# Kernel optimization log

Hardware: AMD Instinct MI355X
Metric: run time of the kernel (lower is better)

The kernel has to match this reference:

```python
import jax, jax.numpy as jnp
import numpy as np

N = 50000
E = 800000
IN_DIM = 6
HID = 32
HEADS = 2
NEG_SLOPE = 0.2


def setup_inputs() -> dict:
    key = jax.random.key(0)
    ks = jax.random.split(key, 12)
    x = jax.random.normal(ks[0], (N, IN_DIM), dtype=jnp.float32)
    edge_index = jax.random.randint(ks[1], (2, E), 0, N, dtype=jnp.int64)
    s = 0.1
    W1 = jax.random.normal(ks[2], (IN_DIM, HEADS * HID), jnp.float32) * s
    a_src1 = jax.random.normal(ks[3], (HEADS, HID), jnp.float32) * s
    a_dst1 = jax.random.normal(ks[4], (HEADS, HID), jnp.float32) * s
    b1 = jnp.zeros((HEADS * HID,), jnp.float32)
    W2 = jax.random.normal(ks[5], (HEADS * HID, HID), jnp.float32) * s
    a_src2 = jax.random.normal(ks[6], (1, HID), jnp.float32) * s
    a_dst2 = jax.random.normal(ks[7], (1, HID), jnp.float32) * s
    b2 = jnp.zeros((HID,), jnp.float32)
    Wout = jax.random.normal(ks[8], (HID, 1), jnp.float32) * s
    bout = jnp.zeros((1,), jnp.float32)
    return {"x": x, "edge_index": edge_index, "W1": W1, "a_src1": a_src1,
            "a_dst1": a_dst1, "b1": b1, "W2": W2, "a_src2": a_src2,
            "a_dst2": a_dst2, "b2": b2, "Wout": Wout, "bout": bout}


def gat_conv(x, src, dst, n, W, a_src, a_dst, b, heads, out_ch, concat):
    # x: [N, F_in]; src/dst: [E'] (self-loops already appended)
    h = (x @ W).reshape(n, heads, out_ch)              # [N, H, C]
    alpha_s = jnp.sum(h * a_src, axis=-1)              # [N, H]
    alpha_d = jnp.sum(h * a_dst, axis=-1)              # [N, H]
    e = jax.nn.leaky_relu(alpha_s[src] + alpha_d[dst], NEG_SLOPE)  # [E', H]
    # segment softmax over incoming edges of each destination node
    m = jax.ops.segment_max(e, dst, num_segments=n)    # [N, H]
    ex = jnp.exp(e - m[dst])
    denom = jax.ops.segment_sum(ex, dst, num_segments=n)
    alpha = ex / denom[dst]                            # [E', H]
    out = jax.ops.segment_sum(alpha[:, :, None] * h[src], dst, num_segments=n)  # [N, H, C]
    out = out.reshape(n, heads * out_ch) if concat else out.mean(axis=1)
    return out + b


def reference(x, edge_index, W1, a_src1, a_dst1, b1, W2, a_src2, a_dst2, b2, Wout, bout):
    n = x.shape[0]
    loops = jnp.arange(n, dtype=edge_index.dtype)
    src = jnp.concatenate([edge_index[0], loops])
    dst = jnp.concatenate([edge_index[1], loops])
    h = jax.nn.relu(gat_conv(x, src, dst, n, W1, a_src1, a_dst1, b1, HEADS, HID, True))
    h = jax.nn.relu(gat_conv(h, src, dst, n, W2, a_src2, a_dst2, b2, 1, HID, False))
    return jax.nn.sigmoid(h @ Wout + bout).squeeze(-1)  # [N]
```

## Files before the change

### kernel.cpp

```cpp
#include <hip/hip_runtime.h>
#include <hip/hip_fp16.h>

#define N_NODES 50000
#define N_EDGES 800000
#define ETOT    (N_EDGES + N_NODES)
#define NEG_SLOPE 0.2f
#define NBIN    ((N_NODES + 255) / 256)
#define CHUNK   4096
#define B_COARSE ((ETOT + CHUNK - 1) / CHUNK)
#define G_NODE1 ((N_NODES + 3) / 4)
#define NG1     (N_NODES / 16)

__device__ __forceinline__ float leaky(float v) {
    return v > 0.f ? v : NEG_SLOPE * v;
}

__device__ __forceinline__ void edge_src_dst(const int* ei, int e, int& src, int& dst) {
    if (e < N_EDGES) { src = ei[e]; dst = ei[N_EDGES + e]; }
    else             { src = dst = e - N_EDGES; }
}

__global__ void k_pre(const float* __restrict__ x, const float* __restrict__ W1,
                      const float* __restrict__ a_src1, const float* __restrict__ a_dst1,
                      float* __restrict__ as1, float* __restrict__ ad1,
                      const int* __restrict__ ei, int* __restrict__ bh) {
    __shared__ int h[NBIN];
    if (blockIdx.x < G_NODE1) {
        int node = blockIdx.x * 4 + (threadIdx.x >> 6);
        if (node >= N_NODES) return;
        int j = threadIdx.x & 63;
        int head = j >> 5;
        float hv = 0.f;
#pragma unroll
        for (int k = 0; k < 6; ++k)
            hv += x[node * 6 + k] * W1[k * 64 + j];
        float s = hv * a_src1[j];
        float d = hv * a_dst1[j];
#pragma unroll
        for (int m = 1; m < 32; m <<= 1) {
            s += __shfl_xor(s, m);
            d += __shfl_xor(d, m);
        }
        if ((j & 31) == 0) {
            as1[node * 2 + head] = s;
            ad1[node * 2 + head] = d;
        }
    } else {
        int b = blockIdx.x - G_NODE1;
        for (int i = threadIdx.x; i < NBIN; i += 256) h[i] = 0;
        __syncthreads();
        int base = b * CHUNK;
        int lim = min(base + CHUNK, ETOT);
        for (int e = base + threadIdx.x; e < lim; e += 256) {
            int s, d; edge_src_dst(ei, e, s, d);
            atomicAdd(&h[d >> 8], 1);
        }
        __syncthreads();
        for (int i = threadIdx.x; i < NBIN; i += 256)
            bh[b * NBIN + i] = h[i];
    }
}

__global__ void k_cscan(int* __restrict__ bh, int* __restrict__ binoff) {
    __shared__ int s[256];
    int t = threadIdx.x;
    int run = 0;
    if (t < NBIN) {
        for (int b = 0; b < B_COARSE; ++b) {
            int v = bh[b * NBIN + t];
            bh[b * NBIN + t] = run;
            run += v;
        }
    }
    int v = (t < NBIN) ? run : 0;
    int x = v;
    s[t] = x;
    __syncthreads();
#pragma unroll
    for (int o = 1; o < 256; o <<= 1) {
        int tt = (t >= o) ? s[t - o] : 0;
        __syncthreads();
        x += tt;
        s[t] = x;
        __syncthreads();
    }
    if (t < NBIN) binoff[t] = x - v;
    if (t == 255) binoff[NBIN] = x;
}

__global__ void k_cscatter(const int* __restrict__ ei, const int* __restrict__ bh,
                           const int* __restrict__ binoff, unsigned* __restrict__ ebin) {
    __shared__ int cur[NBIN];
    for (int i = threadIdx.x; i < NBIN; i += 256)
        cur[i] = bh[blockIdx.x * NBIN + i] + binoff[i];
    __syncthreads();
    int base = blockIdx.x * CHUNK;
    int lim = min(base + CHUNK, ETOT);
    for (int e = base + threadIdx.x; e < lim; e += 256) {
        int s, d; edge_src_dst(ei, e, s, d);
        int pos = atomicAdd(&cur[d >> 8], 1);
        ebin[pos] = ((unsigned)s << 8) | (unsigned)(d & 255);
    }
}

__global__ void k_fine(const unsigned* __restrict__ ebin, const int* __restrict__ binoff,
                       int* __restrict__ rowstart, int* __restrict__ csr_src) {
    __shared__ int h[256];
    __shared__ int cur[256];
    int bin = blockIdx.x;
    int beg = binoff[bin], end = binoff[bin + 1];
    int t = threadIdx.x;
    h[t] = 0;
    __syncthreads();
    for (int i = beg + t; i < end; i += 256)
        atomicAdd(&h[ebin[i] & 255u], 1);
    __syncthreads();
    int v = h[t];
    int x = v;
    cur[t] = x;
    __syncthreads();
#pragma unroll
    for (int o = 1; o < 256; o <<= 1) {
        int tt = (t >= o) ? cur[t - o] : 0;
        __syncthreads();
        x += tt;
        cur[t] = x;
        __syncthreads();
    }
    int start = beg + x - v;
    int node = bin * 256 + t;
    if (node < N_NODES) rowstart[node] = start;
    if (bin == NBIN - 1 && t == 0) rowstart[N_NODES] = ETOT;
    cur[t] = start;
    __syncthreads();
    for (int i = beg + t; i < end; i += 256) {
        unsigned p = ebin[i];
        int pos = atomicAdd(&cur[p & 255u], 1);
        csr_src[pos] = (int)(p >> 8);
    }
}

__global__ void k_gat12(const int* __restrict__ csr_src, const int* __restrict__ rowstart,
                        const float* __restrict__ as1, const float* __restrict__ ad1,
                        const float* __restrict__ x, const float* __restrict__ W1,
                        const float* __restrict__ b1, const float* __restrict__ W2,
                        const float* __restrict__ as_w2, const float* __restrict__ ad_w2,
                        __half* __restrict__ h2h, float* __restrict__ as2,
                        float* __restrict__ ad2) {
    __shared__ float W2s[64 * 32];
    __shared__ float o1s[16 * 66];
    int t = threadIdx.x;
    for (int i = t; i < 64 * 32; i += 256)
        W2s[i] = W2[i];

    int l = t & 15;
    int ln = t >> 4;
    int node = blockIdx.x * 16 + ln;

    float p[4][6];
    float bv[4];
#pragma unroll
    for (int m = 0; m < 4; ++m) {
        int c = l + 16 * m;
#pragma unroll
        for (int k = 0; k < 6; ++k)
            p[m][k] = W1[k * 64 + c];
        bv[m] = b1[c];
    }

    int beg = rowstart[node], end = rowstart[node + 1];
    float2 adv = ((const float2*)ad1)[node];

    float a0 = 0, a1 = 0, a2 = 0, a3 = 0, a4 = 0, a5 = 0;
    float c0 = 0, c1 = 0, c2 = 0, c3 = 0, c4 = 0, c5 = 0;
    float dp0 = 0, dp1 = 0;
    for (int i = beg + l; i < end; i += 16) {
        int s = csr_src[i];
        float2 aa = ((const float2*)as1)[s];
        float w0 = __expf(leaky(aa.x + adv.x));
        float w1 = __expf(leaky(aa.y + adv.y));
        dp0 += w0;
        dp1 += w1;
        const float2* xs = (const float2*)(x + s * 6);
        float2 u = xs[0], v = xs[1], w = xs[2];
        a0 += w0 * u.x; a1 += w0 * u.y; a2 += w0 * v.x;
        a3 += w0 * v.y; a4 += w0 * w.x; a5 += w0 * w.y;
        c0 += w1 * u.x; c1 += w1 * u.y; c2 += w1 * v.x;
        c3 += w1 * v.y; c4 += w1 * w.x; c5 += w1 * w.y;
    }
#pragma unroll
    for (int o = 8; o; o >>= 1) {
        a0 += __shfl_xor(a0, o); a1 += __shfl_xor(a1, o); a2 += __shfl_xor(a2, o);
        a3 += __shfl_xor(a3, o); a4 += __shfl_xor(a4, o); a5 += __shfl_xor(a5, o);
        c0 += __shfl_xor(c0, o); c1 += __shfl_xor(c1, o); c2 += __shfl_xor(c2, o);
        c3 += __shfl_xor(c3, o); c4 += __shfl_xor(c4, o); c5 += __shfl_xor(c5, o);
        dp0 += __shfl_xor(dp0, o); dp1 += __shfl_xor(dp1, o);
    }
    float inv0 = 1.f / dp0;
    float inv1 = 1.f / dp1;
#pragma unroll
    for (int m = 0; m < 4; ++m) {
        float dot;
        if (m < 2)
            dot = a0 * p[m][0] + a1 * p[m][1] + a2 * p[m][2]
                + a3 * p[m][3] + a4 * p[m][4] + a5 * p[m][5];
        else
            dot = c0 * p[m][0] + c1 * p[m][1] + c2 * p[m][2]
                + c3 * p[m][3] + c4 * p[m][4] + c5 * p[m][5];
        float v = dot * (m < 2 ? inv0 : inv1) + bv[m];
        o1s[ln * 66 + l + 16 * m] = v > 0.f ? v : 0.f;
    }
    __syncthreads();

    float h0 = 0.f, h1 = 0.f;
#pragma unroll
    for (int k = 0; k < 64; ++k) {
        float ov = o1s[ln * 66 + k];
        h0 += ov * W2s[k * 32 + l];
        h1 += ov * W2s[k * 32 + l + 16];
    }
    h2h[node * 32 + l] = __float2half(h0);
    h2h[node * 32 + l + 16] = __float2half(h1);
    float s2 = h0 * as_w2[l] + h1 * as_w2[l + 16];
    float d2 = h0 * ad_w2[l] + h1 * ad_w2[l + 16];
#pragma unroll
    for (int o = 8; o; o >>= 1) {
        s2 += __shfl_xor(s2, o);
        d2 += __shfl_xor(d2, o);
    }
    if (l == 0) {
        as2[node] = s2;
        ad2[node] = d2;
    }
}

__global__ void k_gat2(const int* __restrict__ csr_src, const int* __restrict__ rowstart,
                       const float* __restrict__ as2, const float* __restrict__ ad2,
                       const __half2* __restrict__ h2h, const float* __restrict__ b2,
                       const float* __restrict__ Wout, const float* __restrict__ bout,
                       float* __restrict__ out) {
    int node = blockIdx.x * 4 + (threadIdx.x >> 6);
    if (node >= N_NODES) return;
    int j = threadIdx.x & 63;
    int f = j & 15;
    int slot = j >> 4;
    int beg = rowstart[node], end = rowstart[node + 1];
    float adv = ad2[node];

    float accx = 0.f, accy = 0.f, dp = 0.f;
    for (int base = beg; base < end; base += 64) {
        int idx = base + j;
        float w = 0.f;
        int s = 0;
        if (idx < end) {
            s = csr_src[idx];
            w = __expf(leaky(as2[s] + adv));
            dp += w;
        }
        int cnt = min(64, end - base);
        for (int k = 0; k < cnt; k += 4) {
            int   sk = __shfl(s, k + slot);
            float wk = __shfl(w, k + slot);
            float2 hv = __half22float2(h2h[sk * 16 + f]);
            accx += wk * hv.x;
            accy += wk * hv.y;
        }
    }
#pragma unroll
    for (int o = 32; o; o >>= 1)
        dp += __shfl_xor(dp, o);
    accx += __shfl_xor(accx, 16); accy += __shfl_xor(accy, 16);
    accx += __shfl_xor(accx, 32); accy += __shfl_xor(accy, 32);

    float inv = 1.f / dp;
    float vx = accx * inv + b2[2 * f];
    float vy = accy * inv + b2[2 * f + 1];
    vx = vx > 0.f ? vx : 0.f;
    vy = vy > 0.f ? vy : 0.f;
    float t = vx * Wout[2 * f] + vy * Wout[2 * f + 1];
#pragma unroll
    for (int o = 8; o; o >>= 1)
        t += __shfl_xor(t, o);
    if (j == 0)
        out[node] = 1.f / (1.f + __expf(-(t + bout[0])));
}

extern "C" void kernel_launch(void* const* d_in, const int* in_sizes, int n_in,
                              void* d_out, int out_size, void* d_ws, size_t ws_size,
                              hipStream_t stream) {
    const float* x    = (const float*)d_in[0];
    const int*   ei   = (const int*)  d_in[1];
    const float* W1   = (const float*)d_in[2];
    const float* asw1 = (const float*)d_in[3];
    const float* adw1 = (const float*)d_in[4];
    const float* b1   = (const float*)d_in[5];
    const float* W2   = (const float*)d_in[6];
    const float* asw2 = (const float*)d_in[7];
    const float* adw2 = (const float*)d_in[8];
    const float* b2   = (const float*)d_in[9];
    const float* Wout = (const float*)d_in[10];
    const float* bout = (const float*)d_in[11];
    float* out = (float*)d_out;

    char* p = (char*)d_ws;
    auto carve = [&](size_t bytes) {
        void* r = (void*)p;
        p += (bytes + 255) & ~size_t(255);
        return r;
    };
    __half*   h2h      = (__half*)  carve((size_t)N_NODES * 32 * 2);
    float*    as1      = (float*)   carve((size_t)N_NODES * 2 * 4);
    float*    ad1      = (float*)   carve((size_t)N_NODES * 2 * 4);
    float*    as2      = (float*)   carve((size_t)N_NODES * 4);
    float*    ad2      = (float*)   carve((size_t)N_NODES * 4);
    int*      bh       = (int*)     carve((size_t)B_COARSE * NBIN * 4);
    int*      binoff   = (int*)     carve((size_t)(NBIN + 1) * 4);
    unsigned* ebin     = (unsigned*)carve((size_t)ETOT * 4);
    int*      rowstart = (int*)     carve((size_t)(N_NODES + 1) * 4);
    int*      csr_src  = (int*)     carve((size_t)ETOT * 4);

    const int TB = 256;

    k_pre     <<<G_NODE1 + B_COARSE, TB, 0, stream>>>(x, W1, asw1, adw1, as1, ad1, ei, bh);
    k_cscan   <<<1, TB, 0, stream>>>(bh, binoff);
    k_cscatter<<<B_COARSE, TB, 0, stream>>>(ei, bh, binoff, ebin);
    k_fine    <<<NBIN, TB, 0, stream>>>(ebin, binoff, rowstart, csr_src);

    k_gat12<<<NG1, TB, 0, stream>>>(csr_src, rowstart, as1, ad1, x, W1, b1,
                                    W2, asw2, adw2, h2h, as2, ad2);

    k_gat2 <<<(N_NODES + 3) / 4, TB, 0, stream>>>(csr_src, rowstart, as2, ad2,
                                                  (const __half2*)h2h, b2, Wout, bout, out);
}
```

Measured before the change: 98.66 us.

## Pack src attention and features into 32-byte records; unroll edge gather loops

k_pre now writes each node's two layer-1 source attention scores and its six input features into one 8-float record. This lets k_gat12 fetch everything it needs per neighbour with two float4 loads instead of separate as1 and x loads. The edge loops in k_gat12 and k_gat2 are unrolled by two so more independent gathers are in flight, and the k_cscan loop gets an unroll pragma. The cost is a slightly larger intermediate buffer and extra predicated work on the tail iteration.

After: 106.4 us. +7.8%, slower.

```diff
diff --git a/kernel.cpp b/kernel.cpp
--- a/kernel.cpp
+++ b/kernel.cpp
@@ -22,7 +22,7 @@
 
 __global__ void k_pre(const float* __restrict__ x, const float* __restrict__ W1,
                       const float* __restrict__ a_src1, const float* __restrict__ a_dst1,
-                      float* __restrict__ as1, float* __restrict__ ad1,
+                      float* __restrict__ xs1, float* __restrict__ ad1,
                       const int* __restrict__ ei, int* __restrict__ bh) {
     __shared__ int h[NBIN];
     if (blockIdx.x < G_NODE1) {
@@ -42,9 +42,11 @@
             d += __shfl_xor(d, m);
         }
         if ((j & 31) == 0) {
-            as1[node * 2 + head] = s;
+            xs1[node * 8 + head] = s;
             ad1[node * 2 + head] = d;
         }
+        if (j >= 2 && j < 8)
+            xs1[node * 8 + j] = x[node * 6 + (j - 2)];
     } else {
         int b = blockIdx.x - G_NODE1;
         for (int i = threadIdx.x; i < NBIN; i += 256) h[i] = 0;
@@ -66,6 +68,7 @@
     int t = threadIdx.x;
     int run = 0;
     if (t < NBIN) {
+#pragma unroll 4
         for (int b = 0; b < B_COARSE; ++b) {
             int v = bh[b * NBIN + t];
             bh[b * NBIN + t] = run;
@@ -141,12 +144,11 @@
 }
 
 __global__ void k_gat12(const int* __restrict__ csr_src, const int* __restrict__ rowstart,
-                        const float* __restrict__ as1, const float* __restrict__ ad1,
-                        const float* __restrict__ x, const float* __restrict__ W1,
-                        const float* __restrict__ b1, const float* __restrict__ W2,
-                        const float* __restrict__ as_w2, const float* __restrict__ ad_w2,
-                        __half* __restrict__ h2h, float* __restrict__ as2,
-                        float* __restrict__ ad2) {
+                        const float* __restrict__ xs1, const float* __restrict__ ad1,
+                        const float* __restrict__ W1, const float* __restrict__ b1,
+                        const float* __restrict__ W2, const float* __restrict__ as_w2,
+                        const float* __restrict__ ad_w2, __half* __restrict__ h2h,
+                        float* __restrict__ as2, float* __restrict__ ad2) {
     __shared__ float W2s[64 * 32];
     __shared__ float o1s[16 * 66];
     int t = threadIdx.x;
@@ -174,19 +176,27 @@
     float a0 = 0, a1 = 0, a2 = 0, a3 = 0, a4 = 0, a5 = 0;
     float c0 = 0, c1 = 0, c2 = 0, c3 = 0, c4 = 0, c5 = 0;
     float dp0 = 0, dp1 = 0;
-    for (int i = beg + l; i < end; i += 16) {
-        int s = csr_src[i];
-        float2 aa = ((const float2*)as1)[s];
-        float w0 = __expf(leaky(aa.x + adv.x));
-        float w1 = __expf(leaky(aa.y + adv.y));
-        dp0 += w0;
-        dp1 += w1;
-        const float2* xs = (const float2*)(x + s * 6);
-        float2 u = xs[0], v = xs[1], w = xs[2];
-        a0 += w0 * u.x; a1 += w0 * u.y; a2 += w0 * v.x;
-        a3 += w0 * v.y; a4 += w0 * w.x; a5 += w0 * w.y;
-        c0 += w1 * u.x; c1 += w1 * u.y; c2 += w1 * v.x;
-        c3 += w1 * v.y; c4 += w1 * w.x; c5 += w1 * w.y;
+    for (int i = beg + l; i < end; i += 32) {
+        int i1 = i + 16;
+        bool has1 = i1 < end;
+        int s0 = csr_src[i];
+        int s1 = has1 ? csr_src[i1] : s0;
+        const float4* x0p = (const float4*)(xs1 + (size_t)s0 * 8);
+        const float4* x1p = (const float4*)(xs1 + (size_t)s1 * 8);
+        float4 A0 = x0p[0], B0 = x0p[1];
+        float4 A1 = x1p[0], B1 = x1p[1];
+        float w00 = __expf(leaky(A0.x + adv.x));
+        float w01 = __expf(leaky(A0.y + adv.y));
+        float w10 = has1 ? __expf(leaky(A1.x + adv.x)) : 0.f;
+        float w11 = has1 ? __expf(leaky(A1.y + adv.y)) : 0.f;
+        dp0 += w00 + w10;
+        dp1 += w01 + w11;
+        a0 += w00 * A0.z + w10 * A1.z; a1 += w00 * A0.w + w10 * A1.w;
+        a2 += w00 * B0.x + w10 * B1.x; a3 += w00 * B0.y + w10 * B1.y;
+        a4 += w00 * B0.z + w10 * B1.z; a5 += w00 * B0.w + w10 * B1.w;
+        c0 += w01 * A0.z + w11 * A1.z; c1 += w01 * A0.w + w11 * A1.w;
+        c2 += w01 * B0.x + w11 * B1.x; c3 += w01 * B0.y + w11 * B1.y;
+        c4 += w01 * B0.z + w11 * B1.z; c5 += w01 * B0.w + w11 * B1.w;
     }
 #pragma unroll
     for (int o = 8; o; o >>= 1) {
@@ -258,12 +268,15 @@
             dp += w;
         }
         int cnt = min(64, end - base);
-        for (int k = 0; k < cnt; k += 4) {
-            int   sk = __shfl(s, k + slot);
-            float wk = __shfl(w, k + slot);
-            float2 hv = __half22float2(h2h[sk * 16 + f]);
-            accx += wk * hv.x;
-            accy += wk * hv.y;
+        for (int k = 0; k < cnt; k += 8) {
+            int   sk0 = __shfl(s, k + slot);
+            float wk0 = __shfl(w, k + slot);
+            int   sk1 = __shfl(s, k + 4 + slot);
+            float wk1 = __shfl(w, k + 4 + slot);
+            float2 h0 = __half22float2(h2h[sk0 * 16 + f]);
+            float2 h1 = __half22float2(h2h[sk1 * 16 + f]);
+            accx += wk0 * h0.x + wk1 * h1.x;
+            accy += wk0 * h0.y + wk1 * h1.y;
         }
     }
 #pragma unroll
@@ -308,8 +321,8 @@
         p += (bytes + 255) & ~size_t(255);
         return r;
     };
+    float*    xs1      = (float*)   carve((size_t)N_NODES * 8 * 4);
     __half*   h2h      = (__half*)  carve((size_t)N_NODES * 32 * 2);
-    float*    as1      = (float*)   carve((size_t)N_NODES * 2 * 4);
     float*    ad1      = (float*)   carve((size_t)N_NODES * 2 * 4);
     float*    as2      = (float*)   carve((size_t)N_NODES * 4);
     float*    ad2      = (float*)   carve((size_t)N_NODES * 4);
@@ -321,12 +334,12 @@
 
     const int TB = 256;
 
-    k_pre     <<<G_NODE1 + B_COARSE, TB, 0, stream>>>(x, W1, asw1, adw1, as1, ad1, ei, bh);
+    k_pre     <<<G_NODE1 + B_COARSE, TB, 0, stream>>>(x, W1, asw1, adw1, xs1, ad1, ei, bh);
     k_cscan   <<<1, TB, 0, stream>>>(bh, binoff);
     k_cscatter<<<B_COARSE, TB, 0, stream>>>(ei, bh, binoff, ebin);
     k_fine    <<<NBIN, TB, 0, stream>>>(ebin, binoff, rowstart, csr_src);
 
-    k_gat12<<<NG1, TB, 0, stream>>>(csr_src, rowstart, as1, ad1, x, W1, b1,
+    k_gat12<<<NG1, TB, 0, stream>>>(csr_src, rowstart, xs1, ad1, W1, b1,
                                     W2, asw2, adw2, h2h, as2, ad2);
 
     k_gat2 <<<(N_NODES + 3) / 4, TB, 0, stream>>>(csr_src, rowstart, as2, ad2,
```

## Parallelize coarse histogram scan across bins with a two-kernel scan

Applied to the files above, without the earlier changes.

The single-block scan, which walked all coarse chunks serially per bin, is split into two kernels. The first runs one block per bin and scans across chunks in parallel, writing per-bin totals. The second does the small exclusive scan over bin totals. This removes a long serial dependency chain of global loads (about 208 per thread) in one block, at the cost of an extra kernel launch and strided global accesses.

New measurement: 96.40 us, median of 3. -2.3%, faster.

```diff
diff --git a/kernel.cpp b/kernel.cpp
--- a/kernel.cpp
+++ b/kernel.cpp
@@ -61,18 +61,30 @@
     }
 }
 
-__global__ void k_cscan(int* __restrict__ bh, int* __restrict__ binoff) {
+__global__ void k_cscan_a(int* __restrict__ bh, int* __restrict__ bintot) {
+    __shared__ int s[256];
+    int bin = blockIdx.x;
+    int t = threadIdx.x;
+    int v = (t < B_COARSE) ? bh[t * NBIN + bin] : 0;
+    int x = v;
+    s[t] = x;
+    __syncthreads();
+#pragma unroll
+    for (int o = 1; o < 256; o <<= 1) {
+        int tt = (t >= o) ? s[t - o] : 0;
+        __syncthreads();
+        x += tt;
+        s[t] = x;
+        __syncthreads();
+    }
+    if (t < B_COARSE) bh[t * NBIN + bin] = x - v;
+    if (t == 255) bintot[bin] = x;
+}
+
+__global__ void k_cscan_b(const int* __restrict__ bintot, int* __restrict__ binoff) {
     __shared__ int s[256];
     int t = threadIdx.x;
-    int run = 0;
-    if (t < NBIN) {
-        for (int b = 0; b < B_COARSE; ++b) {
-            int v = bh[b * NBIN + t];
-            bh[b * NBIN + t] = run;
-            run += v;
-        }
-    }
-    int v = (t < NBIN) ? run : 0;
+    int v = (t < NBIN) ? bintot[t] : 0;
     int x = v;
     s[t] = x;
     __syncthreads();
@@ -314,6 +326,7 @@
     float*    as2      = (float*)   carve((size_t)N_NODES * 4);
     float*    ad2      = (float*)   carve((size_t)N_NODES * 4);
     int*      bh       = (int*)     carve((size_t)B_COARSE * NBIN * 4);
+    int*      bintot   = (int*)     carve((size_t)NBIN * 4);
     int*      binoff   = (int*)     carve((size_t)(NBIN + 1) * 4);
     unsigned* ebin     = (unsigned*)carve((size_t)ETOT * 4);
     int*      rowstart = (int*)     carve((size_t)(N_NODES + 1) * 4);
@@ -322,7 +335,8 @@
     const int TB = 256;
 
     k_pre     <<<G_NODE1 + B_COARSE, TB, 0, stream>>>(x, W1, asw1, adw1, as1, ad1, ei, bh);
-    k_cscan   <<<1, TB, 0, stream>>>(bh, binoff);
+    k_cscan_a <<<NBIN, TB, 0, stream>>>(bh, bintot);
+    k_cscan_b <<<1, TB, 0, stream>>>(bintot, binoff);
     k_cscatter<<<B_COARSE, TB, 0, stream>>>(ei, bh, binoff, ebin);
     k_fine    <<<NBIN, TB, 0, stream>>>(ebin, binoff, rowstart, csr_src);
 
```
